# Kernel tuning notes

Measured on AMD Instinct MI355X. Metric: run time of the kernel, lower is better.

The kernel has to match this reference:

```python
import jax, jax.numpy as jnp
import numpy as np

STATE_DIM = 1024
INPUT_DIM = 1024
BATCH = 8192


def setup_inputs() -> dict:
    key = jax.random.key(0)
    ks = jax.random.split(key, 7)
    # Kaiming-uniform-ish init like torch Linear
    bx = 1.0 / np.sqrt(INPUT_DIM)
    bh = 1.0 / np.sqrt(STATE_DIM)
    return {
        "x": jax.random.normal(ks[0], (BATCH, INPUT_DIM), jnp.float32),
        "prevh": jax.random.normal(ks[1], (BATCH, STATE_DIM), jnp.float32),
        "prevc": jax.random.normal(ks[2], (BATCH, STATE_DIM), jnp.float32),
        "Wx": jax.random.uniform(ks[3], (INPUT_DIM, 4 * STATE_DIM), jnp.float32, -bx, bx),
        "bx": jax.random.uniform(ks[4], (4 * STATE_DIM,), jnp.float32, -bx, bx),
        "Wh": jax.random.uniform(ks[5], (STATE_DIM, 4 * STATE_DIM), jnp.float32, -bh, bh),
    }


def reference(x, prevh, prevc, Wx, bx, Wh):
    # stacked gate pre-activations: [B, 4*state_dim]
    stacked = x @ Wx + bx + prevh @ Wh
    i_bar, f_bar, o_bar, g_bar = jnp.split(stacked, 4, axis=1)
    i = jax.nn.sigmoid(i_bar)
    f = jax.nn.sigmoid(f_bar)
    o = jax.nn.sigmoid(o_bar)
    g = jnp.tanh(g_bar)
    nextc = prevc * f + g * i
    nexth = jnp.tanh(nextc) * o
    return (nexth, nextc)
```

## Files before the change

kernel.cpp:

```cpp
#include <hip/hip_runtime.h>
#include <hip/hip_bf16.h>


#define BATCH   8192
#define SDIM    1024
#define KDIM    2048
#define NT      32

typedef __attribute__((ext_vector_type(8))) short s16x8;
typedef __attribute__((ext_vector_type(4))) float f32x4;

__device__ __forceinline__ void gload16(const void* g, void* l) {
    __builtin_amdgcn_global_load_lds((const __attribute__((address_space(1))) void*)g,
                                     (__attribute__((address_space(3))) void*)l,
                                     16, 0, 0);
}

__device__ __forceinline__ float fast_sigmoid(float x) {
    return 1.0f / (1.0f + __expf(-x));
}
__device__ __forceinline__ float fast_tanh(float v) {
    float a = fabsf(v);
    float e = __expf(-2.0f * a);
    float t = (1.0f - e) / (1.0f + e);
    return copysignf(t, v);
}

__global__ void convA(const float* __restrict__ x, const float* __restrict__ h,
                      __hip_bfloat16* __restrict__ A) {
    int t = blockIdx.x * blockDim.x + threadIdx.x;
    int e = t << 3;
    int b = e >> 11;
    int k = e & 2047;
    const float* src = (k < 1024) ? (x + (size_t)b * 1024 + k)
                                  : (h + (size_t)b * 1024 + (k - 1024));
    float4 v0 = *(const float4*)(src);
    float4 v1 = *(const float4*)(src + 4);
    union { __hip_bfloat16 b[8]; s16x8 v; } u;
    u.b[0] = __float2bfloat16(v0.x); u.b[1] = __float2bfloat16(v0.y);
    u.b[2] = __float2bfloat16(v0.z); u.b[3] = __float2bfloat16(v0.w);
    u.b[4] = __float2bfloat16(v1.x); u.b[5] = __float2bfloat16(v1.y);
    u.b[6] = __float2bfloat16(v1.z); u.b[7] = __float2bfloat16(v1.w);
    *(s16x8*)(A + e) = u.v;
}

__global__ void convW2(const float* __restrict__ Wx, const float* __restrict__ Wh,
                       __hip_bfloat16* __restrict__ Wt2) {
    int tid  = blockIdx.x * blockDim.x + threadIdx.x;
    int lane = tid & 63;
    int r    = tid >> 6;
    int kfg  = r & 7;
    int g    = kfg >> 1;
    int kf   = kfg & 1;
    int r2   = r >> 3;
    int kt   = r2 & 31;
    int r3   = r2 >> 5;
    int wc   = r3 & 3;
    int ntl  = r3 >> 2;
    int n     = g * 1024 + ntl * 64 + wc * 16 + (lane & 15);
    int kbase = kt * 64 + kf * 32 + (lane >> 4) * 8;
    const float* src = (kbase < 1024) ? (Wx + (size_t)kbase * 4096 + n)
                                      : (Wh + (size_t)(kbase - 1024) * 4096 + n);
    union { __hip_bfloat16 b[8]; s16x8 v; } u;
#pragma unroll
    for (int e = 0; e < 8; ++e)
        u.b[e] = __float2bfloat16(src[(size_t)e * 4096]);
    *(s16x8*)((char*)Wt2 + (size_t)tid * 16) = u.v;
}

__global__ __launch_bounds__(512, 2) void lstm_gemm(
    const __hip_bfloat16* __restrict__ A,
    const __hip_bfloat16* __restrict__ Wt2,
    const float* __restrict__ bx,
    const float* __restrict__ prevc,
    float* __restrict__ outh,
    float* __restrict__ outc)
{
    __shared__ __align__(16) char lds[65536];

    const int tid  = threadIdx.x;
    const int lane = tid & 63;
    const int w    = tid >> 6;
    const int wr   = w >> 2;
    const int wc   = w & 3;
    const int l15  = lane & 15;

    const int bid = blockIdx.x;
    const int xcd = bid & 7, j = bid >> 3;
    const int mt = (xcd >> 1) * 8 + (j & 7);
    const int nt = (xcd & 1) * 8 + (j >> 3);
    const int m0 = mt * 256, S0 = nt * 64;

    const int scol = ((lane & 7) ^ (lane >> 3)) << 3;
    const __hip_bfloat16* Ag = A + (size_t)m0 * KDIM;

    auto SA = [&](int tt, int p) {
        char* dst = lds + (2 * (tt & 1) + p) * 16384 + w * 1024;
        const __hip_bfloat16* src =
            Ag + (size_t)(p * 128 + w * 8 + (lane >> 3)) * KDIM + tt * 64 + scol;
        gload16(src, dst);
        gload16(src + (size_t)64 * KDIM, dst + 8192);
    };

    const char* wb = (const char*)Wt2 + ((size_t)(nt * 4 + wc) * 32) * 8192
                   + (size_t)lane * 16;

    f32x4 acc[8][4];
#pragma unroll
    for (int m = 0; m < 8; ++m)
#pragma unroll
        for (int g = 0; g < 4; ++g)
            acc[m][g] = (f32x4)0.0f;

    s16x8 bfA[4][2], bfB[4][2];
    s16x8 afX[2][2], afY[2][2];

#define LOADB(BF, T)                                                      \
    _Pragma("unroll")                                                     \
    for (int g = 0; g < 4; ++g)                                           \
        _Pragma("unroll")                                                 \
        for (int kf = 0; kf < 2; ++kf)                                    \
            BF[g][kf] = *(const s16x8*)(wb + (size_t)(T) * 8192           \
                                           + (g * 2 + kf) * 1024);

    SA(0, 0); SA(0, 1);
    LOADB(bfA, 0);
    asm volatile("s_waitcnt vmcnt(8)" ::: "memory");
    __builtin_amdgcn_s_barrier();
    __builtin_amdgcn_sched_barrier(0);

    const int swz0 = (((lane >> 4))     ^ (lane & 7)) << 4;
    const int swz1 = (((lane >> 4) | 4) ^ (lane & 7)) << 4;

#define LGKM(n)                                             \
    asm volatile("s_waitcnt lgkmcnt(" #n ")" ::: "memory"); \
    __builtin_amdgcn_sched_barrier(0);

#define RD2(AF, r0)                                                           \
    _Pragma("unroll")                                                         \
    for (int mm = 0; mm < 2; ++mm) {                                          \
        AF[mm][0] = *(const s16x8*)(as + (((r0) + mm) * 16 + l15) * 128 + swz0);\
        AF[mm][1] = *(const s16x8*)(as + (((r0) + mm) * 16 + l15) * 128 + swz1);\
    }

#define MB(AF, BF, mb)                                                        \
    __builtin_amdgcn_s_setprio(1);                                            \
    _Pragma("unroll")                                                         \
    for (int kf = 0; kf < 2; ++kf)                                            \
        _Pragma("unroll")                                                     \
        for (int mm = 0; mm < 2; ++mm)                                        \
            _Pragma("unroll")                                                 \
            for (int g = 0; g < 4; ++g)                                       \
                acc[(mb) + mm][g] = __builtin_amdgcn_mfma_f32_16x16x32_bf16(  \
                    AF[mm][kf], BF[g][kf], acc[(mb) + mm][g], 0, 0, 0);       \
    __builtin_amdgcn_s_setprio(0);

#define TILE(T, BFC, BFN)                                                     \
    {                                                                         \
        const char* as = lds + (2 * ((T) & 1) + wr) * 16384;                  \
        if ((T) + 1 < NT) {                                                   \
            LOADB(BFN, (T) + 1);                                              \
            SA((T) + 1, 0); SA((T) + 1, 1);                                   \
        }                                                                     \
        RD2(afX, 0);                                                          \
        RD2(afY, 2);                                                          \
        LGKM(4); MB(afX, BFC, 0);                                             \
        RD2(afX, 4);                                                          \
        LGKM(4); MB(afY, BFC, 2);                                             \
        RD2(afY, 6);                                                          \
        LGKM(4); MB(afX, BFC, 4);                                             \
        LGKM(0); MB(afY, BFC, 6);                                             \
        asm volatile("s_waitcnt vmcnt(0)" ::: "memory");                      \
        __builtin_amdgcn_s_barrier();                                         \
        __builtin_amdgcn_sched_barrier(0);                                    \
    }

    for (int t = 0; t < NT; t += 2) {
        TILE(t,     bfA, bfB);
        TILE(t + 1, bfB, bfA);
    }
#undef TILE
#undef MB
#undef RD2
#undef LGKM
#undef LOADB

    const int st  = S0 + wc * 16 + l15;
    const float b_i = bx[st];
    const float b_f = bx[1024 + st];
    const float b_o = bx[2048 + st];
    const float b_g = bx[3072 + st];
    const int rbase = m0 + wr * 128 + (lane >> 4) * 4;

#pragma unroll
    for (int m = 0; m < 8; ++m) {
#pragma unroll
        for (int q = 0; q < 4; ++q) {
            int row = rbase + m * 16 + q;
            float ib = acc[m][0][q] + b_i;
            float fb = acc[m][1][q] + b_f;
            float ob = acc[m][2][q] + b_o;
            float gb = acc[m][3][q] + b_g;
            float ig = fast_sigmoid(ib);
            float fg = fast_sigmoid(fb);
            float og = fast_sigmoid(ob);
            float gg = fast_tanh(gb);
            float pc = prevc[(size_t)row * SDIM + st];
            float nc = pc * fg + gg * ig;
            float nh = fast_tanh(nc) * og;
            outh[(size_t)row * SDIM + st] = nh;
            outc[(size_t)row * SDIM + st] = nc;
        }
    }
}

extern "C" void kernel_launch(void* const* d_in, const int* in_sizes, int n_in,
                              void* d_out, int out_size, void* d_ws, size_t ws_size,
                              hipStream_t stream) {
    const float* x     = (const float*)d_in[0];
    const float* prevh = (const float*)d_in[1];
    const float* prevc = (const float*)d_in[2];
    const float* Wx    = (const float*)d_in[3];
    const float* bx    = (const float*)d_in[4];
    const float* Wh    = (const float*)d_in[5];

    __hip_bfloat16* Abf = (__hip_bfloat16*)d_ws;
    __hip_bfloat16* Wt2 = Abf + (size_t)BATCH * KDIM;

    float* outh = (float*)d_out;
    float* outc = outh + (size_t)BATCH * SDIM;

    hipLaunchKernelGGL(convA, dim3(8192), dim3(256), 0, stream, x, prevh, Abf);
    hipLaunchKernelGGL(convW2, dim3(4096), dim3(256), 0, stream, Wx, Wh, Wt2);
    hipLaunchKernelGGL(lstm_gemm, dim3(512), dim3(512), 0, stream,
                       Abf, Wt2, bx, prevc, outh, outc);
}
```

Measured before the change: 162.1 us.

## Pre-swizzle A into MFMA fragment layout and load operands directly from global

```diff
diff --git a/kernel.cpp b/kernel.cpp
--- a/kernel.cpp
+++ b/kernel.cpp
@@ -5,16 +5,10 @@
 #define BATCH   8192
 #define SDIM    1024
 #define KDIM    2048
-#define NT      32
+#define NHS     64
 
 typedef __attribute__((ext_vector_type(8))) short s16x8;
 typedef __attribute__((ext_vector_type(4))) float f32x4;
-
-__device__ __forceinline__ void gload16(const void* g, void* l) {
-    __builtin_amdgcn_global_load_lds((const __attribute__((address_space(1))) void*)g,
-                                     (__attribute__((address_space(3))) void*)l,
-                                     16, 0, 0);
-}
 
 __device__ __forceinline__ float fast_sigmoid(float x) {
     return 1.0f / (1.0f + __expf(-x));
@@ -26,22 +20,40 @@
     return copysignf(t, v);
 }
 
-__global__ void convA(const float* __restrict__ x, const float* __restrict__ h,
-                      __hip_bfloat16* __restrict__ A) {
-    int t = blockIdx.x * blockDim.x + threadIdx.x;
-    int e = t << 3;
-    int b = e >> 11;
-    int k = e & 2047;
-    const float* src = (k < 1024) ? (x + (size_t)b * 1024 + k)
-                                  : (h + (size_t)b * 1024 + (k - 1024));
-    float4 v0 = *(const float4*)(src);
-    float4 v1 = *(const float4*)(src + 4);
-    union { __hip_bfloat16 b[8]; s16x8 v; } u;
-    u.b[0] = __float2bfloat16(v0.x); u.b[1] = __float2bfloat16(v0.y);
-    u.b[2] = __float2bfloat16(v0.z); u.b[3] = __float2bfloat16(v0.w);
-    u.b[4] = __float2bfloat16(v1.x); u.b[5] = __float2bfloat16(v1.y);
-    u.b[6] = __float2bfloat16(v1.z); u.b[7] = __float2bfloat16(v1.w);
-    *(s16x8*)(A + e) = u.v;
+__global__ void convA2(const float* __restrict__ x, const float* __restrict__ h,
+                       __hip_bfloat16* __restrict__ Af) {
+    __shared__ float tile[128][68];
+    const int blk = blockIdx.x;
+    const int kt  = blk & 31;
+    const int mw  = blk >> 5;
+    const int row0 = mw * 128;
+    const int k0   = kt * 64;
+    const int t = threadIdx.x;
+
+    const int r  = t >> 1;
+    const int kc = (t & 1) * 32;
+    const float* src = (k0 < 1024)
+        ? (x + (size_t)(row0 + r) * 1024 + k0 + kc)
+        : (h + (size_t)(row0 + r) * 1024 + (k0 - 1024) + kc);
+#pragma unroll
+    for (int j = 0; j < 8; ++j)
+        *(float4*)&tile[r][kc + j * 4] = *(const float4*)(src + j * 4);
+    __syncthreads();
+
+#pragma unroll
+    for (int q = 0; q < 4; ++q) {
+        int w    = t + q * 256;
+        int lane = w & 63;
+        int kf   = (w >> 6) & 1;
+        int m    = w >> 7;
+        int rr   = m * 16 + (lane & 15);
+        int cc   = kf * 32 + (lane >> 4) * 8;
+        union { __hip_bfloat16 b[8]; s16x8 v; } u;
+#pragma unroll
+        for (int e = 0; e < 8; ++e)
+            u.b[e] = __float2bfloat16(tile[rr][cc + e]);
+        *(s16x8*)(Af + ((size_t)blk * 1024 + w) * 8) = u.v;
+    }
 }
 
 __global__ void convW2(const float* __restrict__ Wx, const float* __restrict__ Wh,
@@ -69,15 +81,13 @@
 }
 
 __global__ __launch_bounds__(512, 2) void lstm_gemm(
-    const __hip_bfloat16* __restrict__ A,
+    const __hip_bfloat16* __restrict__ Af,
     const __hip_bfloat16* __restrict__ Wt2,
     const float* __restrict__ bx,
     const float* __restrict__ prevc,
     float* __restrict__ outh,
     float* __restrict__ outc)
 {
-    __shared__ __align__(16) char lds[65536];
-
     const int tid  = threadIdx.x;
     const int lane = tid & 63;
     const int w    = tid >> 6;
@@ -86,24 +96,15 @@
     const int l15  = lane & 15;
 
     const int bid = blockIdx.x;
-    const int xcd = bid & 7, j = bid >> 3;
-    const int mt = (xcd >> 1) * 8 + (j & 7);
-    const int nt = (xcd & 1) * 8 + (j >> 3);
+    const int xcd = bid & 7, jj = bid >> 3;
+    const int mt = (xcd >> 1) * 8 + (jj & 7);
+    const int nt = (xcd & 1) * 8 + (jj >> 3);
     const int m0 = mt * 256, S0 = nt * 64;
 
-    const int scol = ((lane & 7) ^ (lane >> 3)) << 3;
-    const __hip_bfloat16* Ag = A + (size_t)m0 * KDIM;
-
-    auto SA = [&](int tt, int p) {
-        char* dst = lds + (2 * (tt & 1) + p) * 16384 + w * 1024;
-        const __hip_bfloat16* src =
-            Ag + (size_t)(p * 128 + w * 8 + (lane >> 3)) * KDIM + tt * 64 + scol;
-        gload16(src, dst);
-        gload16(src + (size_t)64 * KDIM, dst + 8192);
-    };
-
-    const char* wb = (const char*)Wt2 + ((size_t)(nt * 4 + wc) * 32) * 8192
-                   + (size_t)lane * 16;
+    const char* pA = (const char*)Af
+                   + ((size_t)(mt * 2 + wr) * 32) * 16384 + (size_t)lane * 16;
+    const char* pB = (const char*)Wt2
+                   + ((size_t)(nt * 4 + wc) * 32) * 8192 + (size_t)lane * 16;
 
     f32x4 acc[8][4];
 #pragma unroll
@@ -112,78 +113,50 @@
         for (int g = 0; g < 4; ++g)
             acc[m][g] = (f32x4)0.0f;
 
-    s16x8 bfA[4][2], bfB[4][2];
-    s16x8 afX[2][2], afY[2][2];
-
-#define LOADB(BF, T)                                                      \
-    _Pragma("unroll")                                                     \
-    for (int g = 0; g < 4; ++g)                                           \
-        _Pragma("unroll")                                                 \
-        for (int kf = 0; kf < 2; ++kf)                                    \
-            BF[g][kf] = *(const s16x8*)(wb + (size_t)(T) * 8192           \
-                                           + (g * 2 + kf) * 1024);
-
-    SA(0, 0); SA(0, 1);
-    LOADB(bfA, 0);
-    asm volatile("s_waitcnt vmcnt(8)" ::: "memory");
-    __builtin_amdgcn_s_barrier();
-    __builtin_amdgcn_sched_barrier(0);
-
-    const int swz0 = (((lane >> 4))     ^ (lane & 7)) << 4;
-    const int swz1 = (((lane >> 4) | 4) ^ (lane & 7)) << 4;
-
-#define LGKM(n)                                             \
-    asm volatile("s_waitcnt lgkmcnt(" #n ")" ::: "memory"); \
-    __builtin_amdgcn_sched_barrier(0);
-
-#define RD2(AF, r0)                                                           \
-    _Pragma("unroll")                                                         \
-    for (int mm = 0; mm < 2; ++mm) {                                          \
-        AF[mm][0] = *(const s16x8*)(as + (((r0) + mm) * 16 + l15) * 128 + swz0);\
-        AF[mm][1] = *(const s16x8*)(as + (((r0) + mm) * 16 + l15) * 128 + swz1);\
-    }
-
-#define MB(AF, BF, mb)                                                        \
+    s16x8 aX[8], bX[4], aY[8], bY[4];
+
+#define LOADF(AR, BR, S)                                                      \
+    {                                                                         \
+        const char* a_ = pA + (size_t)((S) >> 1) * 16384 + ((S) & 1) * 1024;  \
+        const char* b_ = pB + (size_t)((S) >> 1) * 8192 + ((S) & 1) * 1024;   \
+        _Pragma("unroll")                                                     \
+        for (int m = 0; m < 8; ++m)                                           \
+            AR[m] = *(const s16x8*)(a_ + m * 2048);                           \
+        _Pragma("unroll")                                                     \
+        for (int g = 0; g < 4; ++g)                                           \
+            BR[g] = *(const s16x8*)(b_ + g * 2048);                           \
+    }
+
+#define MF(AR, BR)                                                            \
     __builtin_amdgcn_s_setprio(1);                                            \
     _Pragma("unroll")                                                         \
-    for (int kf = 0; kf < 2; ++kf)                                            \
+    for (int m = 0; m < 8; ++m)                                               \
         _Pragma("unroll")                                                     \
-        for (int mm = 0; mm < 2; ++mm)                                        \
-            _Pragma("unroll")                                                 \
-            for (int g = 0; g < 4; ++g)                                       \
-                acc[(mb) + mm][g] = __builtin_amdgcn_mfma_f32_16x16x32_bf16(  \
-                    AF[mm][kf], BF[g][kf], acc[(mb) + mm][g], 0, 0, 0);       \
+        for (int g = 0; g < 4; ++g)                                           \
+            acc[m][g] = __builtin_amdgcn_mfma_f32_16x16x32_bf16(              \
+                AR[m], BR[g], acc[m][g], 0, 0, 0);                            \
     __builtin_amdgcn_s_setprio(0);
 
-#define TILE(T, BFC, BFN)                                                     \
-    {                                                                         \
-        const char* as = lds + (2 * ((T) & 1) + wr) * 16384;                  \
-        if ((T) + 1 < NT) {                                                   \
-            LOADB(BFN, (T) + 1);                                              \
-            SA((T) + 1, 0); SA((T) + 1, 1);                                   \
-        }                                                                     \
-        RD2(afX, 0);                                                          \
-        RD2(afY, 2);                                                          \
-        LGKM(4); MB(afX, BFC, 0);                                             \
-        RD2(afX, 4);                                                          \
-        LGKM(4); MB(afY, BFC, 2);                                             \
-        RD2(afY, 6);                                                          \
-        LGKM(4); MB(afX, BFC, 4);                                             \
-        LGKM(0); MB(afY, BFC, 6);                                             \
-        asm volatile("s_waitcnt vmcnt(0)" ::: "memory");                      \
-        __builtin_amdgcn_s_barrier();                                         \
-        __builtin_amdgcn_sched_barrier(0);                                    \
-    }
-
-    for (int t = 0; t < NT; t += 2) {
-        TILE(t,     bfA, bfB);
-        TILE(t + 1, bfB, bfA);
-    }
-#undef TILE
-#undef MB
-#undef RD2
-#undef LGKM
-#undef LOADB
+    LOADF(aX, bX, 0);
+    for (int s = 0; s < NHS; s += 2) {
+        LOADF(aY, bY, s + 1);
+        asm volatile("s_waitcnt vmcnt(12)" ::: "memory");
+        __builtin_amdgcn_sched_barrier(0);
+        MF(aX, bX);
+
+        if (s + 2 < NHS) {
+            LOADF(aX, bX, s + 2);
+            asm volatile("s_waitcnt vmcnt(12)" ::: "memory");
+        } else {
+            asm volatile("s_waitcnt vmcnt(0)" ::: "memory");
+        }
+        __builtin_amdgcn_sched_barrier(0);
+        MF(aY, bY);
+
+        __builtin_amdgcn_s_barrier();
+    }
+#undef LOADF
+#undef MF
 
     const int st  = S0 + wc * 16 + l15;
     const float b_i = bx[st];
@@ -224,14 +197,14 @@
     const float* bx    = (const float*)d_in[4];
     const float* Wh    = (const float*)d_in[5];
 
-    __hip_bfloat16* Abf = (__hip_bfloat16*)d_ws;
-    __hip_bfloat16* Wt2 = Abf + (size_t)BATCH * KDIM;
+    __hip_bfloat16* Afr = (__hip_bfloat16*)d_ws;
+    __hip_bfloat16* Wt2 = Afr + (size_t)BATCH * KDIM;
 
     float* outh = (float*)d_out;
     float* outc = outh + (size_t)BATCH * SDIM;
 
-    hipLaunchKernelGGL(convA, dim3(8192), dim3(256), 0, stream, x, prevh, Abf);
+    hipLaunchKernelGGL(convA2, dim3(2048), dim3(256), 0, stream, x, prevh, Afr);
     hipLaunchKernelGGL(convW2, dim3(4096), dim3(256), 0, stream, Wx, Wh, Wt2);
     hipLaunchKernelGGL(lstm_gemm, dim3(512), dim3(512), 0, stream,
-                       Abf, Wt2, bx, prevc, outh, outc);
-}
+                       Afr, Wt2, bx, prevc, outh, outc);
+}
```

Result: slower. 182.0 us (+12.2%).
